# Performance work log

Hardware: AMD Instinct MI355X
Metric: run time of the kernel (lower is better)

## Reference

```python
import jax, jax.numpy as jnp
import numpy as np

NUM_USERS = 100000
NUM_ITEMS = 150000
NUM_BRANDS = 5000
NUM_NODES = NUM_USERS + NUM_ITEMS + NUM_BRANDS
EMBED_DIM = 64
N_LAYERS = 3
NUM_EDGES = 2000000


def setup_inputs() -> dict:
    key = jax.random.key(0)
    k1, k2, k3, k4, k5, k6 = jax.random.split(key, 6)
    # xavier_uniform bound for Embedding weight [n, d]
    def xavier(k, n, d):
        bound = float(np.sqrt(6.0 / (n + d)))
        return jax.random.uniform(k, (n, d), dtype=jnp.float32, minval=-bound, maxval=bound)
    user_emb = xavier(k1, NUM_USERS, EMBED_DIM)
    item_emb = xavier(k2, NUM_ITEMS, EMBED_DIM)
    brand_emb = xavier(k3, NUM_BRANDS, EMBED_DIM)
    adj_rows = jax.random.randint(k4, (NUM_EDGES,), 0, NUM_NODES, dtype=jnp.int32)
    adj_cols = jax.random.randint(k5, (NUM_EDGES,), 0, NUM_NODES, dtype=jnp.int32)
    # normalized adjacency values (positive, small), as in sym-normalized LightGCN adj
    adj_vals = jax.random.uniform(k6, (NUM_EDGES,), dtype=jnp.float32) * 0.1
    return {
        "user_emb": user_emb,
        "item_emb": item_emb,
        "brand_emb": brand_emb,
        "adj_rows": adj_rows,
        "adj_cols": adj_cols,
        "adj_vals": adj_vals,
    }


def _spmm(rows, cols, vals, x):
    # y[r] = sum_{e: rows[e]==r} vals[e] * x[cols[e]]
    msgs = vals[:, None] * x[cols]  # [E, D]
    return jax.ops.segment_sum(msgs, rows, num_segments=NUM_NODES)


def reference(user_emb, item_emb, brand_emb, adj_rows, adj_cols, adj_vals):
    ego = jnp.concatenate([user_emb, item_emb, brand_emb], axis=0)  # [N, D]
    acc = ego  # running sum instead of stack+mean
    for _ in range(N_LAYERS):
        ego = _spmm(adj_rows, adj_cols, adj_vals, ego)
        acc = acc + ego
    final = acc / jnp.float32(N_LAYERS + 1)
    final_user = final[:NUM_USERS]
    final_item = final[NUM_USERS:NUM_USERS + NUM_ITEMS]
    return (final_user, final_item)
```

## Files before the change

kernel.cpp:

```cpp
#include <hip/hip_runtime.h>

#define NUSER 100000
#define NITEM 150000
#define NBRAND 5000
#define NNODES (NUSER + NITEM + NBRAND)
#define DIM 64
#define NOUTROWS (NUSER + NITEM)

#define BINSHIFT 10
#define NBINS ((NNODES + (1 << BINSHIFT) - 1) >> BINSHIFT)
#define EPB 8192
#define CAP 12288

__device__ __forceinline__ float bf2f(unsigned short u) {
    union { unsigned int i; float f; } c;
    c.i = ((unsigned int)u) << 16;
    return c.f;
}
__device__ __forceinline__ unsigned short f2bf(float f) {
    union { float f; unsigned int i; } c;
    c.f = f;
    unsigned int r = c.i + 0x7FFFu + ((c.i >> 16) & 1u);
    return (unsigned short)(r >> 16);
}

__global__ __launch_bounds__(256) void lgcn_binA(const int* __restrict__ rows,
                                                 const int* __restrict__ cols,
                                                 const float* __restrict__ vals,
                                                 int* __restrict__ binCnt,
                                                 int2* __restrict__ binned,
                                                 int nedges) {
    __shared__ int hist[NBINS];
    __shared__ int base[NBINS];
    for (int i = threadIdx.x; i < NBINS; i += 256) hist[i] = 0;
    __syncthreads();
    int beg = blockIdx.x * EPB;
    int end = beg + EPB;
    if (end > nedges) end = nedges;
    for (int e = beg + threadIdx.x; e < end; e += 256) {
        atomicAdd(&hist[rows[e] >> BINSHIFT], 1);
    }
    __syncthreads();
    for (int i = threadIdx.x; i < NBINS; i += 256) {
        int h = hist[i];
        base[i] = h ? (i * CAP + atomicAdd(&binCnt[i], h)) : 0;
        hist[i] = 0;
    }
    __syncthreads();
    for (int e = beg + threadIdx.x; e < end; e += 256) {
        int r = rows[e];
        int b = r >> BINSHIFT;
        int pos = base[b] + atomicAdd(&hist[b], 1);
        int2 p;
        p.x = ((r & ((1 << BINSHIFT) - 1)) << 18) | cols[e];
        p.y = __float_as_int(vals[e]);
        binned[pos] = p;
    }
}

__global__ __launch_bounds__(256) void lgcn_binscan(const int* __restrict__ binCnt,
                                                    int* __restrict__ binScan,
                                                    int* __restrict__ rowptr, int nedges) {
    __shared__ int lds[256];
    int t = threadIdx.x;
    int v = (t < NBINS) ? binCnt[t] : 0;
    lds[t] = v;
    __syncthreads();
    for (int off = 1; off < 256; off <<= 1) {
        int s = (t >= off) ? lds[t - off] : 0;
        __syncthreads();
        lds[t] += s;
        __syncthreads();
    }
    if (t < NBINS) binScan[t] = lds[t] - v;
    if (t == 0) rowptr[NNODES] = nedges;
}

__global__ __launch_bounds__(256) void lgcn_binB(const int* __restrict__ binCnt,
                                                 const int* __restrict__ binScan,
                                                 const int2* __restrict__ binned,
                                                 int2* __restrict__ colval,
                                                 int* __restrict__ rowptr) {
    __shared__ int lhist[1024];
    __shared__ int lcur[1024];
    __shared__ int part[256];
    int b = blockIdx.x;
    int t = threadIdx.x;
    int cnt = binCnt[b];
    int gbase = binScan[b];
    int rbeg = b << BINSHIFT;
    int nrows = NNODES - rbeg;
    if (nrows > 1024) nrows = 1024;
    #pragma unroll
    for (int k = 0; k < 4; ++k) lhist[t + 256 * k] = 0;
    __syncthreads();
    const int2* bsrc = binned + (size_t)b * CAP;
    for (int e = t; e < cnt; e += 256) {
        atomicAdd(&lhist[bsrc[e].x >> 18], 1);
    }
    __syncthreads();
    int h0 = lhist[4 * t + 0];
    int h1 = lhist[4 * t + 1];
    int h2 = lhist[4 * t + 2];
    int h3 = lhist[4 * t + 3];
    int tot = h0 + h1 + h2 + h3;
    part[t] = tot;
    __syncthreads();
    for (int off = 1; off < 256; off <<= 1) {
        int v = (t >= off) ? part[t - off] : 0;
        __syncthreads();
        part[t] += v;
        __syncthreads();
    }
    int c0 = gbase + part[t] - tot;
    int c1 = c0 + h0;
    int c2 = c1 + h1;
    int c3 = c2 + h2;
    lcur[4 * t + 0] = c0;
    lcur[4 * t + 1] = c1;
    lcur[4 * t + 2] = c2;
    lcur[4 * t + 3] = c3;
    if (4 * t + 0 < nrows) rowptr[rbeg + 4 * t + 0] = c0;
    if (4 * t + 1 < nrows) rowptr[rbeg + 4 * t + 1] = c1;
    if (4 * t + 2 < nrows) rowptr[rbeg + 4 * t + 2] = c2;
    if (4 * t + 3 < nrows) rowptr[rbeg + 4 * t + 3] = c3;
    __syncthreads();
    for (int e = t; e < cnt; e += 256) {
        int2 p = bsrc[e];
        int lr = p.x >> 18;
        int pos = atomicAdd(&lcur[lr], 1);
        int2 cv;
        cv.x = p.x & 0x3FFFF;
        cv.y = p.y;
        colval[pos] = cv;
    }
}


__global__ __launch_bounds__(256) void lgcn_init(const float4* __restrict__ u,
                                                 const float4* __restrict__ it,
                                                 const float4* __restrict__ br,
                                                 ushort4* __restrict__ x0b) {
    int i = blockIdx.x * blockDim.x + threadIdx.x;
    const int total = NNODES * (DIM / 4);
    if (i >= total) return;
    float4 v;
    if (i < NUSER * (DIM / 4)) {
        v = u[i];
    } else if (i < (NUSER + NITEM) * (DIM / 4)) {
        v = it[i - NUSER * (DIM / 4)];
    } else {
        v = br[i - (NUSER + NITEM) * (DIM / 4)];
    }
    ushort4 o;
    o.x = f2bf(v.x); o.y = f2bf(v.y); o.z = f2bf(v.z); o.w = f2bf(v.w);
    x0b[i] = o;
}

template <bool FINAL>
__global__ __launch_bounds__(256) void lgcn_spmm_csr(const int* __restrict__ row_ptr,
                                                     const int2* __restrict__ colval,
                                                     const ushort4* __restrict__ xb,
                                                     ushort4* __restrict__ yb,
                                                     const float4* __restrict__ u,
                                                     const float4* __restrict__ it,
                                                     const ushort4* __restrict__ y1b,
                                                     const ushort4* __restrict__ y2b,
                                                     float4* __restrict__ out) {
    int t = blockIdx.x * blockDim.x + threadIdx.x;
    int row = t >> 4;
    int l = t & 15;
    if (FINAL) { if (row >= NOUTROWS) return; }
    else       { if (row >= NNODES) return; }
    int beg = row_ptr[row];
    int end = row_ptr[row + 1];
    float4 s = make_float4(0.f, 0.f, 0.f, 0.f);
    int p = beg;
    for (; p + 2 <= end; p += 2) {
        int2 cv0 = colval[p];
        int2 cv1 = colval[p + 1];
        ushort4 a0 = xb[(size_t)cv0.x * (DIM / 4) + l];
        ushort4 a1 = xb[(size_t)cv1.x * (DIM / 4) + l];
        float v0 = __int_as_float(cv0.y);
        float v1 = __int_as_float(cv1.y);
        s.x += v0 * bf2f(a0.x); s.y += v0 * bf2f(a0.y);
        s.z += v0 * bf2f(a0.z); s.w += v0 * bf2f(a0.w);
        s.x += v1 * bf2f(a1.x); s.y += v1 * bf2f(a1.y);
        s.z += v1 * bf2f(a1.z); s.w += v1 * bf2f(a1.w);
    }
    if (p < end) {
        int2 cv = colval[p];
        ushort4 a = xb[(size_t)cv.x * (DIM / 4) + l];
        float v = __int_as_float(cv.y);
        s.x += v * bf2f(a.x); s.y += v * bf2f(a.y);
        s.z += v * bf2f(a.z); s.w += v * bf2f(a.w);
    }
    size_t off = (size_t)row * (DIM / 4) + l;
    if (!FINAL) {
        ushort4 o;
        o.x = f2bf(s.x); o.y = f2bf(s.y); o.z = f2bf(s.z); o.w = f2bf(s.w);
        yb[off] = o;
    } else {
        float4 x0 = (row < NUSER) ? u[off] : it[off - (size_t)NUSER * (DIM / 4)];
        ushort4 a1 = y1b[off];
        ushort4 a2 = y2b[off];
        float4 r;
        r.x = (x0.x + bf2f(a1.x) + bf2f(a2.x) + s.x) * 0.25f;
        r.y = (x0.y + bf2f(a1.y) + bf2f(a2.y) + s.y) * 0.25f;
        r.z = (x0.z + bf2f(a1.z) + bf2f(a2.z) + s.z) * 0.25f;
        r.w = (x0.w + bf2f(a1.w) + bf2f(a2.w) + s.w) * 0.25f;
        out[off] = r;
    }
}


static inline size_t align256(size_t x) { return (x + 255) & ~(size_t)255; }

extern "C" void kernel_launch(void* const* d_in, const int* in_sizes, int n_in,
                              void* d_out, int out_size, void* d_ws, size_t ws_size,
                              hipStream_t stream) {
    const float4* u  = (const float4*)d_in[0];
    const float4* it = (const float4*)d_in[1];
    const float4* br = (const float4*)d_in[2];
    const int*   rows = (const int*)d_in[3];
    const int*   cols = (const int*)d_in[4];
    const float* vals = (const float*)d_in[5];
    const int nedges = in_sizes[3];
    float4* out = (float4*)d_out;

    char* ws = (char*)d_ws;
    size_t o = 0;
    ushort4* x0b   = (ushort4*)(ws + o); o = align256(o + (size_t)NNODES * DIM * 2);
    ushort4* y1b   = (ushort4*)(ws + o); o = align256(o + (size_t)NNODES * DIM * 2);
    ushort4* y2b   = (ushort4*)(ws + o); o = align256(o + (size_t)NNODES * DIM * 2);
    int*   rowptr  = (int*)(ws + o);     o = align256(o + (size_t)(NNODES + 1) * 4);
    int*   binCnt  = (int*)(ws + o);     o = align256(o + 256 * 4);
    int*   binScan = (int*)(ws + o);     o = align256(o + 256 * 4);
    int2*  colval  = (int2*)(ws + o);    o = align256(o + (size_t)nedges * 8);

    int2* binned = (int2*)y1b;

    const int THREADS = 256;
    const int vecTotal = NNODES * (DIM / 4);
    const int vecBlocks = (vecTotal + THREADS - 1) / THREADS;
    const int spmmBlocks = (NNODES * 16 + THREADS - 1) / THREADS;
    const int finalBlocks = (NOUTROWS * 16 + THREADS - 1) / THREADS;
    const int binABlocks = (nedges + EPB - 1) / EPB;

    hipMemsetAsync(binCnt, 0, 256 * 4, stream);
    lgcn_binA<<<binABlocks, THREADS, 0, stream>>>(rows, cols, vals, binCnt, binned, nedges);
    lgcn_binscan<<<1, THREADS, 0, stream>>>(binCnt, binScan, rowptr, nedges);
    lgcn_binB<<<NBINS, THREADS, 0, stream>>>(binCnt, binScan, binned, colval, rowptr);

    lgcn_init<<<vecBlocks, THREADS, 0, stream>>>(u, it, br, x0b);

    lgcn_spmm_csr<false><<<spmmBlocks, THREADS, 0, stream>>>(rowptr, colval, x0b, y1b,
                                                             nullptr, nullptr, nullptr, nullptr, nullptr);
    lgcn_spmm_csr<false><<<spmmBlocks, THREADS, 0, stream>>>(rowptr, colval, y1b, y2b,
                                                             nullptr, nullptr, nullptr, nullptr, nullptr);
    lgcn_spmm_csr<true><<<finalBlocks, THREADS, 0, stream>>>(rowptr, colval, y2b, nullptr,
                                                             u, it, y1b, y2b, out);
}
```

Baseline: 273.1 us.

## Fuse bf16 init into binning kernel and unroll SpMM gather by eight

The embedding-to-bf16 conversion kernel is merged into the edge-binning launch as extra blocks, removing one kernel launch and letting the two independent jobs overlap. The SpMM inner loop now issues eight column/value loads and eight gathers before accumulating, which raises memory-level parallelism per thread. The final layer reads the bf16 copy of layer zero instead of the fp32 inputs, halving that read but adding bf16 rounding to the x0 term. More registers per thread from the unroll may lower occupancy.

```diff
diff --git a/kernel.cpp b/kernel.cpp
--- a/kernel.cpp
+++ b/kernel.cpp
@@ -24,14 +24,35 @@
     return (unsigned short)(r >> 16);
 }
 
-__global__ __launch_bounds__(256) void lgcn_binA(const int* __restrict__ rows,
-                                                 const int* __restrict__ cols,
-                                                 const float* __restrict__ vals,
-                                                 int* __restrict__ binCnt,
-                                                 int2* __restrict__ binned,
-                                                 int nedges) {
+__global__ __launch_bounds__(256) void lgcn_binA_init(const int* __restrict__ rows,
+                                                      const int* __restrict__ cols,
+                                                      const float* __restrict__ vals,
+                                                      int* __restrict__ binCnt,
+                                                      int2* __restrict__ binned,
+                                                      int nedges, int nBinABlocks,
+                                                      const float4* __restrict__ u,
+                                                      const float4* __restrict__ it,
+                                                      const float4* __restrict__ br,
+                                                      ushort4* __restrict__ x0b) {
     __shared__ int hist[NBINS];
     __shared__ int base[NBINS];
+    if (blockIdx.x >= nBinABlocks) {
+        int i = (blockIdx.x - nBinABlocks) * 256 + threadIdx.x;
+        const int total = NNODES * (DIM / 4);
+        if (i >= total) return;
+        float4 v;
+        if (i < NUSER * (DIM / 4)) {
+            v = u[i];
+        } else if (i < (NUSER + NITEM) * (DIM / 4)) {
+            v = it[i - NUSER * (DIM / 4)];
+        } else {
+            v = br[i - (NUSER + NITEM) * (DIM / 4)];
+        }
+        ushort4 o;
+        o.x = f2bf(v.x); o.y = f2bf(v.y); o.z = f2bf(v.z); o.w = f2bf(v.w);
+        x0b[i] = o;
+        return;
+    }
     for (int i = threadIdx.x; i < NBINS; i += 256) hist[i] = 0;
     __syncthreads();
     int beg = blockIdx.x * EPB;
@@ -136,34 +157,12 @@
     }
 }
 
-
-__global__ __launch_bounds__(256) void lgcn_init(const float4* __restrict__ u,
-                                                 const float4* __restrict__ it,
-                                                 const float4* __restrict__ br,
-                                                 ushort4* __restrict__ x0b) {
-    int i = blockIdx.x * blockDim.x + threadIdx.x;
-    const int total = NNODES * (DIM / 4);
-    if (i >= total) return;
-    float4 v;
-    if (i < NUSER * (DIM / 4)) {
-        v = u[i];
-    } else if (i < (NUSER + NITEM) * (DIM / 4)) {
-        v = it[i - NUSER * (DIM / 4)];
-    } else {
-        v = br[i - (NUSER + NITEM) * (DIM / 4)];
-    }
-    ushort4 o;
-    o.x = f2bf(v.x); o.y = f2bf(v.y); o.z = f2bf(v.z); o.w = f2bf(v.w);
-    x0b[i] = o;
-}
-
 template <bool FINAL>
 __global__ __launch_bounds__(256) void lgcn_spmm_csr(const int* __restrict__ row_ptr,
                                                      const int2* __restrict__ colval,
                                                      const ushort4* __restrict__ xb,
                                                      ushort4* __restrict__ yb,
-                                                     const float4* __restrict__ u,
-                                                     const float4* __restrict__ it,
+                                                     const ushort4* __restrict__ x0b,
                                                      const ushort4* __restrict__ y1b,
                                                      const ushort4* __restrict__ y2b,
                                                      float4* __restrict__ out) {
@@ -176,7 +175,37 @@
     int end = row_ptr[row + 1];
     float4 s = make_float4(0.f, 0.f, 0.f, 0.f);
     int p = beg;
-    for (; p + 2 <= end; p += 2) {
+    while (p + 8 <= end) {
+        int2 cv[8];
+        ushort4 a[8];
+        #pragma unroll
+        for (int k = 0; k < 8; ++k) cv[k] = colval[p + k];
+        #pragma unroll
+        for (int k = 0; k < 8; ++k) a[k] = xb[(size_t)cv[k].x * (DIM / 4) + l];
+        #pragma unroll
+        for (int k = 0; k < 8; ++k) {
+            float v = __int_as_float(cv[k].y);
+            s.x += v * bf2f(a[k].x); s.y += v * bf2f(a[k].y);
+            s.z += v * bf2f(a[k].z); s.w += v * bf2f(a[k].w);
+        }
+        p += 8;
+    }
+    if (p + 4 <= end) {
+        int2 cv[4];
+        ushort4 a[4];
+        #pragma unroll
+        for (int k = 0; k < 4; ++k) cv[k] = colval[p + k];
+        #pragma unroll
+        for (int k = 0; k < 4; ++k) a[k] = xb[(size_t)cv[k].x * (DIM / 4) + l];
+        #pragma unroll
+        for (int k = 0; k < 4; ++k) {
+            float v = __int_as_float(cv[k].y);
+            s.x += v * bf2f(a[k].x); s.y += v * bf2f(a[k].y);
+            s.z += v * bf2f(a[k].z); s.w += v * bf2f(a[k].w);
+        }
+        p += 4;
+    }
+    if (p + 2 <= end) {
         int2 cv0 = colval[p];
         int2 cv1 = colval[p + 1];
         ushort4 a0 = xb[(size_t)cv0.x * (DIM / 4) + l];
@@ -187,6 +216,7 @@
         s.z += v0 * bf2f(a0.z); s.w += v0 * bf2f(a0.w);
         s.x += v1 * bf2f(a1.x); s.y += v1 * bf2f(a1.y);
         s.z += v1 * bf2f(a1.z); s.w += v1 * bf2f(a1.w);
+        p += 2;
     }
     if (p < end) {
         int2 cv = colval[p];
@@ -201,14 +231,14 @@
         o.x = f2bf(s.x); o.y = f2bf(s.y); o.z = f2bf(s.z); o.w = f2bf(s.w);
         yb[off] = o;
     } else {
-        float4 x0 = (row < NUSER) ? u[off] : it[off - (size_t)NUSER * (DIM / 4)];
+        ushort4 x0 = x0b[off];
         ushort4 a1 = y1b[off];
         ushort4 a2 = y2b[off];
         float4 r;
-        r.x = (x0.x + bf2f(a1.x) + bf2f(a2.x) + s.x) * 0.25f;
-        r.y = (x0.y + bf2f(a1.y) + bf2f(a2.y) + s.y) * 0.25f;
-        r.z = (x0.z + bf2f(a1.z) + bf2f(a2.z) + s.z) * 0.25f;
-        r.w = (x0.w + bf2f(a1.w) + bf2f(a2.w) + s.w) * 0.25f;
+        r.x = (bf2f(x0.x) + bf2f(a1.x) + bf2f(a2.x) + s.x) * 0.25f;
+        r.y = (bf2f(x0.y) + bf2f(a1.y) + bf2f(a2.y) + s.y) * 0.25f;
+        r.z = (bf2f(x0.z) + bf2f(a1.z) + bf2f(a2.z) + s.z) * 0.25f;
+        r.w = (bf2f(x0.w) + bf2f(a1.w) + bf2f(a2.w) + s.w) * 0.25f;
         out[off] = r;
     }
 }
@@ -248,16 +278,15 @@
     const int binABlocks = (nedges + EPB - 1) / EPB;
 
     hipMemsetAsync(binCnt, 0, 256 * 4, stream);
-    lgcn_binA<<<binABlocks, THREADS, 0, stream>>>(rows, cols, vals, binCnt, binned, nedges);
+    lgcn_binA_init<<<binABlocks + vecBlocks, THREADS, 0, stream>>>(
+        rows, cols, vals, binCnt, binned, nedges, binABlocks, u, it, br, x0b);
     lgcn_binscan<<<1, THREADS, 0, stream>>>(binCnt, binScan, rowptr, nedges);
     lgcn_binB<<<NBINS, THREADS, 0, stream>>>(binCnt, binScan, binned, colval, rowptr);
 
-    lgcn_init<<<vecBlocks, THREADS, 0, stream>>>(u, it, br, x0b);
-
     lgcn_spmm_csr<false><<<spmmBlocks, THREADS, 0, stream>>>(rowptr, colval, x0b, y1b,
-                                                             nullptr, nullptr, nullptr, nullptr, nullptr);
+                                                             nullptr, nullptr, nullptr, nullptr);
     lgcn_spmm_csr<false><<<spmmBlocks, THREADS, 0, stream>>>(rowptr, colval, y1b, y2b,
-                                                             nullptr, nullptr, nullptr, nullptr, nullptr);
+                                                             nullptr, nullptr, nullptr, nullptr);
     lgcn_spmm_csr<true><<<finalBlocks, THREADS, 0, stream>>>(rowptr, colval, y2b, nullptr,
-                                                             u, it, y1b, y2b, out);
-}
+                                                             x0b, y1b, y2b, out);
+}
```

Measured after the change: 238.6 us. 12.6% less time.

## Batch SpMM gathers across two rows, drop bin scan with padded per-bin CSR

Applied to the files above, without the earlier changes.

Each 16-lane group in the SpMM now handles two rows and issues eight colval/feature gathers per row before accumulating, to raise memory-level parallelism on the random gathers. The global bin-scan kernel is removed: CSR now uses a padded per-bin layout, with bins at fixed CAP offsets and RPS row pointers per bin. The binning kernels use 1024-thread blocks with registers holding the row indices. The final layer reads the bf16 copy of x0 instead of the fp32 inputs, which saves bandwidth but lowers the precision of the output. The cost is masked wasted loads on short rows and larger padded workspace arrays.

```diff
diff --git a/kernel.cpp b/kernel.cpp
--- a/kernel.cpp
+++ b/kernel.cpp
@@ -9,8 +9,9 @@
 
 #define BINSHIFT 10
 #define NBINS ((NNODES + (1 << BINSHIFT) - 1) >> BINSHIFT)
-#define EPB 8192
+#define EPB_A 8192
 #define CAP 12288
+#define RPS 1025
 
 __device__ __forceinline__ float bf2f(unsigned short u) {
     union { unsigned int i; float f; } c;
@@ -24,111 +25,82 @@
     return (unsigned short)(r >> 16);
 }
 
-__global__ __launch_bounds__(256) void lgcn_binA(const int* __restrict__ rows,
-                                                 const int* __restrict__ cols,
-                                                 const float* __restrict__ vals,
-                                                 int* __restrict__ binCnt,
-                                                 int2* __restrict__ binned,
-                                                 int nedges) {
+__global__ __launch_bounds__(1024) void lgcn_binA(const int* __restrict__ rows,
+                                                  const int* __restrict__ cols,
+                                                  const float* __restrict__ vals,
+                                                  int* __restrict__ binCnt,
+                                                  int2* __restrict__ binned,
+                                                  int nedges) {
     __shared__ int hist[NBINS];
     __shared__ int base[NBINS];
-    for (int i = threadIdx.x; i < NBINS; i += 256) hist[i] = 0;
-    __syncthreads();
-    int beg = blockIdx.x * EPB;
-    int end = beg + EPB;
+    int t = threadIdx.x;
+    for (int i = t; i < NBINS; i += 1024) hist[i] = 0;
+    __syncthreads();
+    int beg = blockIdx.x * EPB_A;
+    int end = beg + EPB_A;
     if (end > nedges) end = nedges;
-    for (int e = beg + threadIdx.x; e < end; e += 256) {
-        atomicAdd(&hist[rows[e] >> BINSHIFT], 1);
-    }
-    __syncthreads();
-    for (int i = threadIdx.x; i < NBINS; i += 256) {
+    int r[8];
+    #pragma unroll
+    for (int k = 0; k < 8; ++k) {
+        int e = beg + t + k * 1024;
+        r[k] = (e < end) ? rows[e] : -1;
+        if (r[k] >= 0) atomicAdd(&hist[r[k] >> BINSHIFT], 1);
+    }
+    __syncthreads();
+    for (int i = t; i < NBINS; i += 1024) {
         int h = hist[i];
         base[i] = h ? (i * CAP + atomicAdd(&binCnt[i], h)) : 0;
         hist[i] = 0;
     }
     __syncthreads();
-    for (int e = beg + threadIdx.x; e < end; e += 256) {
-        int r = rows[e];
-        int b = r >> BINSHIFT;
-        int pos = base[b] + atomicAdd(&hist[b], 1);
-        int2 p;
-        p.x = ((r & ((1 << BINSHIFT) - 1)) << 18) | cols[e];
-        p.y = __float_as_int(vals[e]);
-        binned[pos] = p;
-    }
-}
-
-__global__ __launch_bounds__(256) void lgcn_binscan(const int* __restrict__ binCnt,
-                                                    int* __restrict__ binScan,
-                                                    int* __restrict__ rowptr, int nedges) {
-    __shared__ int lds[256];
-    int t = threadIdx.x;
-    int v = (t < NBINS) ? binCnt[t] : 0;
-    lds[t] = v;
-    __syncthreads();
-    for (int off = 1; off < 256; off <<= 1) {
-        int s = (t >= off) ? lds[t - off] : 0;
-        __syncthreads();
-        lds[t] += s;
-        __syncthreads();
-    }
-    if (t < NBINS) binScan[t] = lds[t] - v;
-    if (t == 0) rowptr[NNODES] = nedges;
-}
-
-__global__ __launch_bounds__(256) void lgcn_binB(const int* __restrict__ binCnt,
-                                                 const int* __restrict__ binScan,
-                                                 const int2* __restrict__ binned,
-                                                 int2* __restrict__ colval,
-                                                 int* __restrict__ rowptr) {
+    #pragma unroll
+    for (int k = 0; k < 8; ++k) {
+        if (r[k] >= 0) {
+            int e = beg + t + k * 1024;
+            int b = r[k] >> BINSHIFT;
+            int pos = base[b] + atomicAdd(&hist[b], 1);
+            int2 p;
+            p.x = ((r[k] & 1023) << 18) | cols[e];
+            p.y = __float_as_int(vals[e]);
+            binned[pos] = p;
+        }
+    }
+}
+
+__global__ __launch_bounds__(1024) void lgcn_binB(const int* __restrict__ binCnt,
+                                                  const int2* __restrict__ binned,
+                                                  int2* __restrict__ colval,
+                                                  int* __restrict__ rowptr) {
     __shared__ int lhist[1024];
+    __shared__ int part[1024];
     __shared__ int lcur[1024];
-    __shared__ int part[256];
     int b = blockIdx.x;
     int t = threadIdx.x;
     int cnt = binCnt[b];
-    int gbase = binScan[b];
-    int rbeg = b << BINSHIFT;
-    int nrows = NNODES - rbeg;
-    if (nrows > 1024) nrows = 1024;
-    #pragma unroll
-    for (int k = 0; k < 4; ++k) lhist[t + 256 * k] = 0;
+    lhist[t] = 0;
     __syncthreads();
     const int2* bsrc = binned + (size_t)b * CAP;
-    for (int e = t; e < cnt; e += 256) {
+    for (int e = t; e < cnt; e += 1024) {
         atomicAdd(&lhist[bsrc[e].x >> 18], 1);
     }
     __syncthreads();
-    int h0 = lhist[4 * t + 0];
-    int h1 = lhist[4 * t + 1];
-    int h2 = lhist[4 * t + 2];
-    int h3 = lhist[4 * t + 3];
-    int tot = h0 + h1 + h2 + h3;
-    part[t] = tot;
-    __syncthreads();
-    for (int off = 1; off < 256; off <<= 1) {
+    int h = lhist[t];
+    part[t] = h;
+    __syncthreads();
+    for (int off = 1; off < 1024; off <<= 1) {
         int v = (t >= off) ? part[t - off] : 0;
         __syncthreads();
         part[t] += v;
         __syncthreads();
     }
-    int c0 = gbase + part[t] - tot;
-    int c1 = c0 + h0;
-    int c2 = c1 + h1;
-    int c3 = c2 + h2;
-    lcur[4 * t + 0] = c0;
-    lcur[4 * t + 1] = c1;
-    lcur[4 * t + 2] = c2;
-    lcur[4 * t + 3] = c3;
-    if (4 * t + 0 < nrows) rowptr[rbeg + 4 * t + 0] = c0;
-    if (4 * t + 1 < nrows) rowptr[rbeg + 4 * t + 1] = c1;
-    if (4 * t + 2 < nrows) rowptr[rbeg + 4 * t + 2] = c2;
-    if (4 * t + 3 < nrows) rowptr[rbeg + 4 * t + 3] = c3;
-    __syncthreads();
-    for (int e = t; e < cnt; e += 256) {
+    int c = b * CAP + part[t] - h;
+    lcur[t] = c;
+    rowptr[b * RPS + t] = c;
+    if (t == 1023) rowptr[b * RPS + 1024] = b * CAP + cnt;
+    __syncthreads();
+    for (int e = t; e < cnt; e += 1024) {
         int2 p = bsrc[e];
-        int lr = p.x >> 18;
-        int pos = atomicAdd(&lcur[lr], 1);
+        int pos = atomicAdd(&lcur[p.x >> 18], 1);
         int2 cv;
         cv.x = p.x & 0x3FFFF;
         cv.y = p.y;
@@ -158,58 +130,77 @@
 }
 
 template <bool FINAL>
-__global__ __launch_bounds__(256) void lgcn_spmm_csr(const int* __restrict__ row_ptr,
+__global__ __launch_bounds__(256) void lgcn_spmm_csr(const int* __restrict__ rowptr,
                                                      const int2* __restrict__ colval,
                                                      const ushort4* __restrict__ xb,
                                                      ushort4* __restrict__ yb,
-                                                     const float4* __restrict__ u,
-                                                     const float4* __restrict__ it,
+                                                     const ushort4* __restrict__ x0b,
                                                      const ushort4* __restrict__ y1b,
                                                      const ushort4* __restrict__ y2b,
                                                      float4* __restrict__ out) {
     int t = blockIdx.x * blockDim.x + threadIdx.x;
-    int row = t >> 4;
+    int g = t >> 4;
     int l = t & 15;
-    if (FINAL) { if (row >= NOUTROWS) return; }
-    else       { if (row >= NNODES) return; }
-    int beg = row_ptr[row];
-    int end = row_ptr[row + 1];
-    float4 s = make_float4(0.f, 0.f, 0.f, 0.f);
-    int p = beg;
-    for (; p + 2 <= end; p += 2) {
-        int2 cv0 = colval[p];
-        int2 cv1 = colval[p + 1];
-        ushort4 a0 = xb[(size_t)cv0.x * (DIM / 4) + l];
-        ushort4 a1 = xb[(size_t)cv1.x * (DIM / 4) + l];
-        float v0 = __int_as_float(cv0.y);
-        float v1 = __int_as_float(cv1.y);
-        s.x += v0 * bf2f(a0.x); s.y += v0 * bf2f(a0.y);
-        s.z += v0 * bf2f(a0.z); s.w += v0 * bf2f(a0.w);
-        s.x += v1 * bf2f(a1.x); s.y += v1 * bf2f(a1.y);
-        s.z += v1 * bf2f(a1.z); s.w += v1 * bf2f(a1.w);
-    }
-    if (p < end) {
-        int2 cv = colval[p];
-        ushort4 a = xb[(size_t)cv.x * (DIM / 4) + l];
-        float v = __int_as_float(cv.y);
-        s.x += v * bf2f(a.x); s.y += v * bf2f(a.y);
-        s.z += v * bf2f(a.z); s.w += v * bf2f(a.w);
-    }
-    size_t off = (size_t)row * (DIM / 4) + l;
+    int row0 = g * 2;
+    int row1 = row0 + 1;
+    const int LIMIT = FINAL ? NOUTROWS : NNODES;
+    if (row0 >= LIMIT) return;
+    int i0 = (row0 >> BINSHIFT) * RPS + (row0 & 1023);
+    int i1 = (row1 >> BINSHIFT) * RPS + (row1 & 1023);
+    int beg0 = rowptr[i0], end0 = rowptr[i0 + 1];
+    int beg1 = rowptr[i1], end1 = rowptr[i1 + 1];
+    int safe0 = (beg0 < end0) ? beg0 : 0;
+    int safe1 = (beg1 < end1) ? beg1 : 0;
+    float4 s0 = make_float4(0.f, 0.f, 0.f, 0.f);
+    float4 s1 = make_float4(0.f, 0.f, 0.f, 0.f);
+    int p0 = beg0, p1 = beg1;
+    while (p0 < end0 || p1 < end1) {
+        int2 cv0[8], cv1[8];
+        #pragma unroll
+        for (int k = 0; k < 8; ++k) { int q = p0 + k; cv0[k] = colval[q < end0 ? q : safe0]; }
+        #pragma unroll
+        for (int k = 0; k < 8; ++k) { int q = p1 + k; cv1[k] = colval[q < end1 ? q : safe1]; }
+        ushort4 a0[8], a1[8];
+        #pragma unroll
+        for (int k = 0; k < 8; ++k) a0[k] = xb[(size_t)cv0[k].x * (DIM / 4) + l];
+        #pragma unroll
+        for (int k = 0; k < 8; ++k) a1[k] = xb[(size_t)cv1[k].x * (DIM / 4) + l];
+        #pragma unroll
+        for (int k = 0; k < 8; ++k) {
+            float v = (p0 + k < end0) ? __int_as_float(cv0[k].y) : 0.f;
+            s0.x += v * bf2f(a0[k].x); s0.y += v * bf2f(a0[k].y);
+            s0.z += v * bf2f(a0[k].z); s0.w += v * bf2f(a0[k].w);
+        }
+        #pragma unroll
+        for (int k = 0; k < 8; ++k) {
+            float v = (p1 + k < end1) ? __int_as_float(cv1[k].y) : 0.f;
+            s1.x += v * bf2f(a1[k].x); s1.y += v * bf2f(a1[k].y);
+            s1.z += v * bf2f(a1[k].z); s1.w += v * bf2f(a1[k].w);
+        }
+        p0 += 8; p1 += 8;
+    }
+    size_t off0 = (size_t)row0 * (DIM / 4) + l;
+    size_t off1 = (size_t)row1 * (DIM / 4) + l;
     if (!FINAL) {
-        ushort4 o;
-        o.x = f2bf(s.x); o.y = f2bf(s.y); o.z = f2bf(s.z); o.w = f2bf(s.w);
-        yb[off] = o;
+        ushort4 o0, o1;
+        o0.x = f2bf(s0.x); o0.y = f2bf(s0.y); o0.z = f2bf(s0.z); o0.w = f2bf(s0.w);
+        o1.x = f2bf(s1.x); o1.y = f2bf(s1.y); o1.z = f2bf(s1.z); o1.w = f2bf(s1.w);
+        yb[off0] = o0;
+        yb[off1] = o1;
     } else {
-        float4 x0 = (row < NUSER) ? u[off] : it[off - (size_t)NUSER * (DIM / 4)];
-        ushort4 a1 = y1b[off];
-        ushort4 a2 = y2b[off];
-        float4 r;
-        r.x = (x0.x + bf2f(a1.x) + bf2f(a2.x) + s.x) * 0.25f;
-        r.y = (x0.y + bf2f(a1.y) + bf2f(a2.y) + s.y) * 0.25f;
-        r.z = (x0.z + bf2f(a1.z) + bf2f(a2.z) + s.z) * 0.25f;
-        r.w = (x0.w + bf2f(a1.w) + bf2f(a2.w) + s.w) * 0.25f;
-        out[off] = r;
+        ushort4 x00 = x0b[off0], a10 = y1b[off0], a20 = y2b[off0];
+        ushort4 x01 = x0b[off1], a11 = y1b[off1], a21 = y2b[off1];
+        float4 r0, r1;
+        r0.x = (bf2f(x00.x) + bf2f(a10.x) + bf2f(a20.x) + s0.x) * 0.25f;
+        r0.y = (bf2f(x00.y) + bf2f(a10.y) + bf2f(a20.y) + s0.y) * 0.25f;
+        r0.z = (bf2f(x00.z) + bf2f(a10.z) + bf2f(a20.z) + s0.z) * 0.25f;
+        r0.w = (bf2f(x00.w) + bf2f(a10.w) + bf2f(a20.w) + s0.w) * 0.25f;
+        r1.x = (bf2f(x01.x) + bf2f(a11.x) + bf2f(a21.x) + s1.x) * 0.25f;
+        r1.y = (bf2f(x01.y) + bf2f(a11.y) + bf2f(a21.y) + s1.y) * 0.25f;
+        r1.z = (bf2f(x01.z) + bf2f(a11.z) + bf2f(a21.z) + s1.z) * 0.25f;
+        r1.w = (bf2f(x01.w) + bf2f(a11.w) + bf2f(a21.w) + s1.w) * 0.25f;
+        out[off0] = r0;
+        out[off1] = r1;
     }
 }
 
@@ -233,31 +224,28 @@
     ushort4* x0b   = (ushort4*)(ws + o); o = align256(o + (size_t)NNODES * DIM * 2);
     ushort4* y1b   = (ushort4*)(ws + o); o = align256(o + (size_t)NNODES * DIM * 2);
     ushort4* y2b   = (ushort4*)(ws + o); o = align256(o + (size_t)NNODES * DIM * 2);
-    int*   rowptr  = (int*)(ws + o);     o = align256(o + (size_t)(NNODES + 1) * 4);
+    int*   rowptr  = (int*)(ws + o);     o = align256(o + (size_t)NBINS * RPS * 4);
     int*   binCnt  = (int*)(ws + o);     o = align256(o + 256 * 4);
-    int*   binScan = (int*)(ws + o);     o = align256(o + 256 * 4);
-    int2*  colval  = (int2*)(ws + o);    o = align256(o + (size_t)nedges * 8);
+    int2*  colval  = (int2*)(ws + o);    o = align256(o + (size_t)NBINS * CAP * 8);
 
     int2* binned = (int2*)y1b;
 
-    const int THREADS = 256;
     const int vecTotal = NNODES * (DIM / 4);
-    const int vecBlocks = (vecTotal + THREADS - 1) / THREADS;
-    const int spmmBlocks = (NNODES * 16 + THREADS - 1) / THREADS;
-    const int finalBlocks = (NOUTROWS * 16 + THREADS - 1) / THREADS;
-    const int binABlocks = (nedges + EPB - 1) / EPB;
+    const int vecBlocks = (vecTotal + 255) / 256;
+    const int spmmBlocks  = ((NNODES / 2) * 16 + 255) / 256;
+    const int finalBlocks = ((NOUTROWS / 2) * 16 + 255) / 256;
+    const int binABlocks = (nedges + EPB_A - 1) / EPB_A;
 
     hipMemsetAsync(binCnt, 0, 256 * 4, stream);
-    lgcn_binA<<<binABlocks, THREADS, 0, stream>>>(rows, cols, vals, binCnt, binned, nedges);
-    lgcn_binscan<<<1, THREADS, 0, stream>>>(binCnt, binScan, rowptr, nedges);
-    lgcn_binB<<<NBINS, THREADS, 0, stream>>>(binCnt, binScan, binned, colval, rowptr);
-
-    lgcn_init<<<vecBlocks, THREADS, 0, stream>>>(u, it, br, x0b);
-
-    lgcn_spmm_csr<false><<<spmmBlocks, THREADS, 0, stream>>>(rowptr, colval, x0b, y1b,
-                                                             nullptr, nullptr, nullptr, nullptr, nullptr);
-    lgcn_spmm_csr<false><<<spmmBlocks, THREADS, 0, stream>>>(rowptr, colval, y1b, y2b,
-                                                             nullptr, nullptr, nullptr, nullptr, nullptr);
-    lgcn_spmm_csr<true><<<finalBlocks, THREADS, 0, stream>>>(rowptr, colval, y2b, nullptr,
-                                                             u, it, y1b, y2b, out);
-}
+    lgcn_binA<<<binABlocks, 1024, 0, stream>>>(rows, cols, vals, binCnt, binned, nedges);
+    lgcn_binB<<<NBINS, 1024, 0, stream>>>(binCnt, binned, colval, rowptr);
+
+    lgcn_init<<<vecBlocks, 256, 0, stream>>>(u, it, br, x0b);
+
+    lgcn_spmm_csr<false><<<spmmBlocks, 256, 0, stream>>>(rowptr, colval, x0b, y1b,
+                                                         nullptr, nullptr, nullptr, nullptr);
+    lgcn_spmm_csr<false><<<spmmBlocks, 256, 0, stream>>>(rowptr, colval, y1b, y2b,
+                                                         nullptr, nullptr, nullptr, nullptr);
+    lgcn_spmm_csr<true><<<finalBlocks, 256, 0, stream>>>(rowptr, colval, y2b, nullptr,
+                                                         x0b, y1b, y2b, out);
+}
```

Result: faster. 265.9 us (-2.6%).
